# Optimization experiments

Hardware: AMD Instinct MI355X
Metric: run time of the kernel (lower is better)

The kernel has to match this reference:

```python
import jax, jax.numpy as jnp
import numpy as np
import math

B, LQ, LK = 8, 1024, 1024
D_MODEL, NHEAD = 512, 8
DH = D_MODEL // NHEAD
FACTOR = 5
U = FACTOR * int(np.ceil(np.log(LQ)))  # 35: Informer's sample_k == n_top here (L_Q == L_K)


def _ln(x, g, b, eps=1e-5):
    m = x.mean(-1, keepdims=True)
    v = ((x - m) ** 2).mean(-1, keepdims=True)
    return (x - m) / jnp.sqrt(v + eps) * g + b


def _heads(x):  # (B,L,D) -> (B,H,L,Dh)
    Bx, L, _ = x.shape
    return x.reshape(Bx, L, NHEAD, DH).transpose(0, 2, 1, 3)


def _merge(x):  # (B,H,L,Dh) -> (B,L,D)
    Bx, H, L, Dh = x.shape
    return x.transpose(0, 2, 1, 3).reshape(Bx, L, H * Dh)


def _prob_attn(q, k, v, index_sample):
    # Informer ProbAttention, mask_flag=False. q,k,v: (B,H,L,Dh)
    Bx, H, Lq, Dh = q.shape
    Lk = k.shape[2]
    k_samp = k[:, :, index_sample, :]                        # (B,H,Lq,U,Dh) gathered keys
    qk_samp = jnp.einsum('bhld,bhlud->bhlu', q, k_samp)      # sampled scores
    M = qk_samp.max(-1) - qk_samp.sum(-1) / Lk               # sparsity measurement (B,H,Lq)
    _, top = jax.lax.top_k(M, U)                             # (B,H,U) top-u query indices
    q_red = jnp.take_along_axis(q, top[..., None], axis=2)   # (B,H,U,Dh)
    scores = jnp.einsum('bhud,bhkd->bhuk', q_red, k) * (1.0 / math.sqrt(Dh))
    attn = jax.nn.softmax(scores, axis=-1)
    upd = jnp.einsum('bhuk,bhkd->bhud', attn, v)             # (B,H,U,Dh)
    # initial context = mean of V (non-causal branch), then scatter top-u rows
    ctx = jnp.broadcast_to(v.mean(2, keepdims=True), (Bx, H, Lq, Dh))
    bi = jnp.arange(Bx)[:, None, None]
    hi = jnp.arange(H)[None, :, None]
    ctx = ctx.at[bi, hi, top].set(upd)
    return ctx


def _full_attn(q, k, v):
    s = jnp.einsum('bhld,bhsd->bhls', q, k) * (1.0 / math.sqrt(q.shape[-1]))
    a = jax.nn.softmax(s, axis=-1)
    return jnp.einsum('bhls,bhsd->bhld', a, v)


def setup_inputs():
    key = jax.random.key(0)
    ks = jax.random.split(key, 40)
    d = {}
    d['tgt'] = jax.random.normal(ks[0], (B, LQ, D_MODEL), jnp.float32)
    d['memory'] = jax.random.normal(ks[1], (B, LK, D_MODEL), jnp.float32)
    d['index_sample'] = jax.random.randint(ks[2], (LQ, U), 0, LK)
    i = 3
    for pre in ('1', '2'):
        for n in ('q', 'k', 'v', 'o'):
            d['w%s%s' % (n, pre)] = jax.random.normal(ks[i], (D_MODEL, D_MODEL), jnp.float32) * 0.02
            d['b%s%s' % (n, pre)] = jnp.zeros((D_MODEL,), jnp.float32)
            i += 1
    d['conv1_w'] = jax.random.normal(ks[i], (D_MODEL, 4 * D_MODEL), jnp.float32) * 0.02; i += 1
    d['conv1_b'] = jnp.zeros((4 * D_MODEL,), jnp.float32)
    d['conv2_w'] = jax.random.normal(ks[i], (4 * D_MODEL, D_MODEL), jnp.float32) * 0.02; i += 1
    d['conv2_b'] = jnp.zeros((D_MODEL,), jnp.float32)
    for n in ('ln1', 'ln2', 'ln3'):
        d[n + '_g'] = jnp.ones((D_MODEL,), jnp.float32)
        d[n + '_b'] = jnp.zeros((D_MODEL,), jnp.float32)
    return d


def reference(tgt, memory, index_sample, wq1, bq1, wk1, bk1, wv1, bv1, wo1, bo1,
              wq2, bq2, wk2, bk2, wv2, bv2, wo2, bo2,
              conv1_w, conv1_b, conv2_w, conv2_b,
              ln1_g, ln1_b, ln2_g, ln2_b, ln3_g, ln3_b):
    # dropout layers are identity (eval mode)
    x = tgt
    q = _heads(x @ wq1 + bq1)
    k = _heads(x @ wk1 + bk1)
    v = _heads(x @ wv1 + bv1)
    xn = _merge(_prob_attn(q, k, v, index_sample)) @ wo1 + bo1   # ProbSparse self-attn
    x = _ln(x + xn, ln1_g, ln1_b)                                # norm_enc1, with residual
    q = _heads(x @ wq2 + bq2)
    k = _heads(memory @ wk2 + bk2)
    v = _heads(memory @ wv2 + bv2)
    x = _merge(_full_attn(q, k, v)) @ wo2 + bo2                  # full cross-attn (no residual, per source)
    y = x = _ln(x, ln2_g, ln2_b)                                 # norm_enc2
    y = jax.nn.relu(y @ conv1_w + conv1_b) @ conv2_w + conv2_b   # conv1x1 FFN
    return _ln(x + y, ln3_g, ln3_b)                              # norm_enc3
```

## Files before the change

kernel.cpp:

```cpp
#include <hip/hip_runtime.h>
#include <hip/hip_bf16.h>
#include <cstdint>

constexpr int Bb  = 8;
constexpr int Ls  = 1024;
constexpr int DM  = 512;
constexpr int NH  = 8;
constexpr int DHd = 64;
constexpr int MR  = Bb * Ls;
constexpr int ZH  = Bb * NH;

typedef __attribute__((ext_vector_type(8))) short short8v;
typedef __attribute__((ext_vector_type(4))) short short4v;
typedef __attribute__((ext_vector_type(4))) float floatx4;

__device__ inline short f2bf(float x) {
  __hip_bfloat16 h = __float2bfloat16(x);
  return *reinterpret_cast<short*>(&h);
}
__device__ inline float bf2f(short s) {
  return __uint_as_float(((uint32_t)(uint16_t)s) << 16);
}

#define GLOAD_LDS16(g, l)                                                        \
  __builtin_amdgcn_global_load_lds(                                              \
      (const __attribute__((address_space(1))) void*)(g),                        \
      (__attribute__((address_space(3))) void*)(l), 16, 0, 0)

template<int MODE, int RELU>
__global__ __launch_bounds__(256) void k_gemm_mfma(
    const __hip_bfloat16* __restrict__ A, const __hip_bfloat16* __restrict__ Wt,
    const float* __restrict__ bias, const float* __restrict__ bias1,
    const float* __restrict__ bias2,
    void* __restrict__ Cout, void* __restrict__ aux1, void* __restrict__ aux2,
    void* __restrict__ aux3,
    int M, int N, int K)
{
  __shared__ __hip_bfloat16 As[128 * 32];
  __shared__ __hip_bfloat16 Bs[128 * 32];
  const int tid = threadIdx.x;
  const int w = tid >> 6, lane = tid & 63;
  const int wr = w >> 1, wc = w & 1;
  const int bm = blockIdx.x * 128, bn = blockIdx.y * 128;
  const int lrow = lane >> 2;
  const int lcol = (lane & 3) * 8;
  const int fr = lane & 15;
  const int fco = (lane >> 4) * 8;
  const short* Ash = (const short*)As;
  const short* Bsh = (const short*)Bs;

  const __hip_bfloat16* Asrc = A;
  if (MODE == 12 && bn >= 512) Asrc = (const __hip_bfloat16*)aux3;

  const int ksl = K / gridDim.z;
  const int kb0 = blockIdx.z * ksl;

  floatx4 acc[4][4] = {};
  for (int k0 = kb0; k0 < kb0 + ksl; k0 += 32) {
#pragma unroll
    for (int i = 0; i < 2; ++i) {
      const int chunk = w * 2 + i;
      GLOAD_LDS16(Asrc + (size_t)(bm + chunk * 16 + lrow) * K + k0 + lcol,
                  As + chunk * 512);
      GLOAD_LDS16(Wt + (size_t)(bn + chunk * 16 + lrow) * K + k0 + lcol,
                  Bs + chunk * 512);
    }
    __syncthreads();
    short8v a[4], b[4];
#pragma unroll
    for (int mi = 0; mi < 4; ++mi)
      a[mi] = *(const short8v*)(Ash + (wr * 64 + mi * 16 + fr) * 32 + fco);
#pragma unroll
    for (int ni = 0; ni < 4; ++ni)
      b[ni] = *(const short8v*)(Bsh + (wc * 64 + ni * 16 + fr) * 32 + fco);
#pragma unroll
    for (int mi = 0; mi < 4; ++mi)
#pragma unroll
      for (int ni = 0; ni < 4; ++ni)
        acc[mi][ni] = __builtin_amdgcn_mfma_f32_16x16x32_bf16(
            a[mi], b[ni], acc[mi][ni], 0, 0, 0);
    __syncthreads();
  }
#pragma unroll
  for (int ni = 0; ni < 4; ++ni) {
    const int cn = bn + wc * 64 + ni * 16 + fr;
    float bv = 0.f;
    if (MODE == 10 || MODE == 12) {
      const float* bp = (cn < 512) ? bias : (cn < 1024 ? bias1 : bias2);
      bv = bp[cn & 511];
    } else if (MODE != 20) {
      bv = bias[cn];
    }
#pragma unroll
    for (int mi = 0; mi < 4; ++mi) {
#pragma unroll
      for (int j = 0; j < 4; ++j) {
        const int rm = bm + wr * 64 + mi * 16 + (lane >> 4) * 4 + j;
        float v = acc[mi][ni][j] + bv;
        if (RELU) v = fmaxf(v, 0.f);
        if (MODE == 1) {
          ((__hip_bfloat16*)Cout)[(size_t)rm * N + cn] = __float2bfloat16(v);
        } else if (MODE == 10) {
          const int sel = cn >> 9, c = cn & 511;
          if (sel == 2) {
            ((float*)aux2)[(size_t)rm * 512 + c] = v;
          } else {
            const int bb = rm >> 10, l = rm & 1023, hh = c >> 6, dd = c & 63;
            const size_t ci = (((size_t)(bb * 8 + hh)) * 1024 + l) * 64 + dd;
            float* base = sel ? (float*)aux1 : (float*)Cout;
            base[ci] = v;
            __hip_bfloat16* bb16 = (__hip_bfloat16*)aux3 +
                                   (sel ? (size_t)ZH * Ls * 64 : 0);
            bb16[ci] = __float2bfloat16(v);
          }
        } else if (MODE == 12) {
          const int sel = cn >> 9, c = cn & 511;
          if (sel == 0) {
            ((__hip_bfloat16*)Cout)[(size_t)rm * 512 + c] =
                __float2bfloat16(v * 0.125f);
          } else if (sel == 1) {
            const int cs = (c & ~63) | ((c & 63) ^ ((rm & 7) << 3));
            ((__hip_bfloat16*)aux1)[(size_t)rm * 512 + cs] = __float2bfloat16(v);
          } else {
            const int bb = rm >> 10, l = rm & 1023, hh = c >> 6, dd = c & 63;
            ((__hip_bfloat16*)aux2)[(size_t)((bb * 8 + hh) * 64 + dd) * 1024 +
                                    (l ^ ((dd & 7) << 3))] = __float2bfloat16(v);
          }
        } else if (MODE == 20) {
          float* pz = (float*)(blockIdx.z == 0 ? Cout :
                      blockIdx.z == 1 ? aux1 :
                      blockIdx.z == 2 ? aux2 : aux3);
          pz[(size_t)rm * N + cn] = v;
        }
      }
    }
  }
}

__global__ __launch_bounds__(512) void k_flash2(
    const __hip_bfloat16* __restrict__ Qb,
    const __hip_bfloat16* __restrict__ Kb,
    const __hip_bfloat16* __restrict__ Vt,
    __hip_bfloat16* __restrict__ O)
{
  __shared__ __hip_bfloat16 Ks[2][64 * 64];
  __shared__ __hip_bfloat16 Vs[2][64 * 64];
  __shared__ __hip_bfloat16 Ps[8 * 16 * 72];
  const int tid = threadIdx.x, w = tid >> 6, lane = tid & 63;
  const int g = lane >> 4, r = lane & 15;
  const int z = blockIdx.y, b = z >> 3, h = z & 7;
  const int q0 = blockIdx.x * 128 + w * 16;
  __hip_bfloat16* Pw = Ps + w * 16 * 72;

  const int srow = w * 8 + (lane >> 3);
  const int sseg = lane & 7;

  const short8v qf0 = *(const short8v*)(Qb + (size_t)(b * Ls + q0 + r) * DM + h * DHd + g * 8);
  const short8v qf1 = *(const short8v*)(Qb + (size_t)(b * Ls + q0 + r) * DM + h * DHd + 32 + g * 8);

  floatx4 oacc[4] = {};
  float m_run = -1e30f, l_run = 0.f;

  GLOAD_LDS16(Kb + (size_t)(b * Ls + srow) * DM + h * DHd + sseg * 8, &Ks[0][w * 512]);
  GLOAD_LDS16(Vt + ((size_t)z * DHd + srow) * Ls + sseg * 8, &Vs[0][w * 512]);
  asm volatile("s_waitcnt vmcnt(0)" ::: "memory");
  __builtin_amdgcn_s_barrier();

  int cur = 0;
  for (int t = 0; t < 16; ++t) {
    if (t + 1 < 16) {
      GLOAD_LDS16(Kb + (size_t)(b * Ls + (t + 1) * 64 + srow) * DM + h * DHd + sseg * 8,
                  &Ks[cur ^ 1][w * 512]);
      GLOAD_LDS16(Vt + ((size_t)z * DHd + srow) * Ls + (t + 1) * 64 + sseg * 8,
                  &Vs[cur ^ 1][w * 512]);
    }
    const __hip_bfloat16* Kc = Ks[cur];
    const __hip_bfloat16* Vc = Vs[cur];
    float sv[4][4];
    float tmax = -1e30f;
    __builtin_amdgcn_s_setprio(1);
#pragma unroll
    for (int kt = 0; kt < 4; ++kt) {
      const int key = kt * 16 + r, sw = key & 7;
      short8v a0 = *(const short8v*)(Kc + key * 64 + ((g ^ sw) * 8));
      short8v a1 = *(const short8v*)(Kc + key * 64 + (((4 + g) ^ sw) * 8));
      floatx4 c = {};
      c = __builtin_amdgcn_mfma_f32_16x16x32_bf16(a0, qf0, c, 0, 0, 0);
      c = __builtin_amdgcn_mfma_f32_16x16x32_bf16(a1, qf1, c, 0, 0, 0);
#pragma unroll
      for (int j = 0; j < 4; ++j) {
        float x = c[j];
        sv[kt][j] = x;
        tmax = fmaxf(tmax, x);
      }
    }
    __builtin_amdgcn_s_setprio(0);
    tmax = fmaxf(tmax, __shfl_xor(tmax, 16));
    tmax = fmaxf(tmax, __shfl_xor(tmax, 32));
    float m_new;
    if (__all(tmax <= m_run + 8.0f)) {
      m_new = m_run;
    } else {
      m_new = fmaxf(m_run, tmax);
      const float fac = __expf(m_run - m_new);
      float fj[4];
#pragma unroll
      for (int j = 0; j < 4; ++j) fj[j] = __shfl(fac, (lane & 48) | (g * 4 + j));
#pragma unroll
      for (int ct = 0; ct < 4; ++ct)
#pragma unroll
        for (int j = 0; j < 4; ++j) oacc[ct][j] *= fj[j];
      l_run *= fac;
    }
    float psum = 0.f;
#pragma unroll
    for (int kt = 0; kt < 4; ++kt) {
      short4v pk;
#pragma unroll
      for (int j = 0; j < 4; ++j) {
        float p = __expf(sv[kt][j] - m_new);
        psum += p;
        pk[j] = f2bf(p);
      }
      *(short4v*)(Pw + r * 72 + kt * 16 + g * 4) = pk;
    }
    psum += __shfl_xor(psum, 16);
    psum += __shfl_xor(psum, 32);
    l_run += psum;
    m_run = m_new;
    const short8v pa0 = *(const short8v*)(Pw + r * 72 + g * 8);
    const short8v pa1 = *(const short8v*)(Pw + r * 72 + 32 + g * 8);
    __builtin_amdgcn_s_setprio(1);
#pragma unroll
    for (int ct = 0; ct < 4; ++ct) {
      const int d = ct * 16 + r, sw = d & 7;
      short8v v0 = *(const short8v*)(Vc + d * 64 + ((g ^ sw) * 8));
      short8v v1 = *(const short8v*)(Vc + d * 64 + (((4 + g) ^ sw) * 8));
      oacc[ct] = __builtin_amdgcn_mfma_f32_16x16x32_bf16(pa0, v0, oacc[ct], 0, 0, 0);
      oacc[ct] = __builtin_amdgcn_mfma_f32_16x16x32_bf16(pa1, v1, oacc[ct], 0, 0, 0);
    }
    __builtin_amdgcn_s_setprio(0);
    asm volatile("s_waitcnt vmcnt(0)" ::: "memory");
    __builtin_amdgcn_s_barrier();
    cur ^= 1;
  }
  float li[4];
#pragma unroll
  for (int j = 0; j < 4; ++j)
    li[j] = 1.0f / __shfl(l_run, (lane & 48) | (g * 4 + j));
#pragma unroll
  for (int ct = 0; ct < 4; ++ct)
#pragma unroll
    for (int j = 0; j < 4; ++j)
      O[(size_t)(b * Ls + q0 + g * 4 + j) * DM + h * DHd + ct * 16 + r] =
          __float2bfloat16(oacc[ct][j] * li[j]);
}

struct CvtArgs { const float* s[12]; __hip_bfloat16* d[12]; };
__global__ __launch_bounds__(256) void k_cvt_all(CvtArgs a)
{
  const int bid = blockIdx.x, tid = threadIdx.x;
  if (bid < 8192) {
    const size_t half = (size_t)MR * DM / 4;
    size_t i = (size_t)bid * 256 + tid;
    const float* in = a.s[10]; __hip_bfloat16* out = a.d[10];
    if (i >= half) { i -= half; in = a.s[11]; out = a.d[11]; }
    float4 v = *reinterpret_cast<const float4*>(in + i * 4);
    short4v o;
    o.x = f2bf(v.x); o.y = f2bf(v.y); o.z = f2bf(v.z); o.w = f2bf(v.w);
    *reinterpret_cast<short4v*>(out + i * 4) = o;
    return;
  }
  __shared__ float t[32][33];
  const int wb = bid - 8192;
  int widx, K, N, kblk, nblk;
  if (wb < 2048) {
    widx = wb >> 8; const int w2 = wb & 255;
    K = 512; N = 512; kblk = w2 & 15; nblk = w2 >> 4;
  } else if (wb < 3072) {
    widx = 8; const int w2 = wb - 2048;
    K = 512; N = 2048; kblk = w2 & 15; nblk = w2 >> 4;
  } else {
    widx = 9; const int w2 = wb - 3072;
    K = 2048; N = 512; kblk = w2 & 63; nblk = w2 >> 6;
  }
  const float* W = a.s[widx];
  __hip_bfloat16* Wt = a.d[widx];
  const int k0 = kblk * 32, n0 = nblk * 32;
  const int r = tid >> 3, c = (tid & 7) * 4;
  float4 v = *reinterpret_cast<const float4*>(W + (size_t)(k0 + r) * N + n0 + c);
  t[r][c + 0] = v.x; t[r][c + 1] = v.y; t[r][c + 2] = v.z; t[r][c + 3] = v.w;
  __syncthreads();
  short4v o;
  o.x = f2bf(t[c + 0][r]); o.y = f2bf(t[c + 1][r]);
  o.z = f2bf(t[c + 2][r]); o.w = f2bf(t[c + 3][r]);
  *reinterpret_cast<short4v*>(Wt + (size_t)(n0 + r) * K + k0 + c) = o;
}

__global__ __launch_bounds__(256) void k_probflash(
    const float* __restrict__ Qz, const float* __restrict__ Kz,
    const float* __restrict__ Vm, const int* __restrict__ top,
    float* __restrict__ Op, float* __restrict__ Ml, float* __restrict__ Ll,
    int U)
{
  __shared__ float Qs[DHd][64 + 4];
  __shared__ float Ks[DHd][64 + 4];
  __shared__ float Vs[64][64];
  const int bid = blockIdx.x;
  const int swz = (bid & 7) * ((16 * ZH) >> 3) + (bid >> 3);
  const int kc = swz & 15, z = swz >> 4, b = z >> 3, h = z & 7;
  const int tid = threadIdx.x;
  const int k0 = kc * 64;
#pragma unroll
  for (int i = 0; i < 4; ++i) {
    const int idx = tid + (i << 8);
    const int r = idx >> 4, c4 = (idx & 15) << 2;
    int u = r; if (u >= U) u = U - 1;
    const int qr = top[z * U + u];
    float4 q4 = *reinterpret_cast<const float4*>(Qz + ((size_t)z * Ls + qr) * 64 + c4);
    Qs[c4 + 0][r] = q4.x; Qs[c4 + 1][r] = q4.y; Qs[c4 + 2][r] = q4.z; Qs[c4 + 3][r] = q4.w;
    float4 k4 = *reinterpret_cast<const float4*>(Kz + ((size_t)z * Ls + k0 + r) * 64 + c4);
    Ks[c4 + 0][r] = k4.x; Ks[c4 + 1][r] = k4.y; Ks[c4 + 2][r] = k4.z; Ks[c4 + 3][r] = k4.w;
    *reinterpret_cast<float4*>(&Vs[r][c4]) =
        *reinterpret_cast<const float4*>(Vm + ((size_t)(b * Ls + k0 + r)) * DM + h * DHd + c4);
  }
  __syncthreads();
  const int mB = (tid >> 4) << 2, nB = (tid & 15) << 2;
  float acc[4][4] = {};
#pragma unroll
  for (int kk = 0; kk < DHd; ++kk) {
    float4 a4 = *reinterpret_cast<const float4*>(&Qs[kk][mB]);
    float4 b4 = *reinterpret_cast<const float4*>(&Ks[kk][nB]);
    const float av[4] = {a4.x, a4.y, a4.z, a4.w};
#pragma unroll
    for (int i = 0; i < 4; ++i) {
      acc[i][0] += av[i] * b4.x; acc[i][1] += av[i] * b4.y;
      acc[i][2] += av[i] * b4.z; acc[i][3] += av[i] * b4.w;
    }
  }
  __syncthreads();
  float (*Ss)[68] = (float (*)[68])Qs;
#pragma unroll
  for (int i = 0; i < 4; ++i) {
    float4 o;
    o.x = acc[i][0] * 0.125f; o.y = acc[i][1] * 0.125f;
    o.z = acc[i][2] * 0.125f; o.w = acc[i][3] * 0.125f;
    *reinterpret_cast<float4*>(&Ss[mB + i][nB]) = o;
  }
  __syncthreads();
  {
    const int row = tid >> 2, q = tid & 3;
    float mx = -1e30f;
#pragma unroll
    for (int j = 0; j < 16; ++j) mx = fmaxf(mx, Ss[row][q * 16 + j]);
    mx = fmaxf(mx, __shfl_xor(mx, 1));
    mx = fmaxf(mx, __shfl_xor(mx, 2));
    float se = 0.f;
#pragma unroll
    for (int j = 0; j < 16; ++j) {
      float p = __expf(Ss[row][q * 16 + j] - mx);
      Ss[row][q * 16 + j] = p;
      se += p;
    }
    se += __shfl_xor(se, 1);
    se += __shfl_xor(se, 2);
    if (q == 0) {
      Ml[((size_t)kc * ZH + z) * 64 + row] = mx;
      Ll[((size_t)kc * ZH + z) * 64 + row] = se;
    }
  }
  __syncthreads();
  const int d = tid & 63, w = tid >> 6;
  float acc2[16] = {};
  for (int k = 0; k < 64; ++k) {
    const float vk = Vs[k][d];
#pragma unroll
    for (int i = 0; i < 16; ++i)
      acc2[i] += Ss[w * 16 + i][k] * vk;
  }
  float* outb = Op + ((size_t)kc * ZH + z) * 4096;
#pragma unroll
  for (int i = 0; i < 16; ++i)
    outb[(w * 16 + i) * 64 + d] = acc2[i];
}

__global__ __launch_bounds__(256) void k_prob_comb(
    const float* __restrict__ Op, const float* __restrict__ Ml,
    const float* __restrict__ Ll, const int* __restrict__ top,
    __hip_bfloat16* __restrict__ ctx, int U)
{
  __shared__ float wsh[16][64];
  __shared__ float Lsh[64];
  const int z = blockIdx.x, b = z >> 3, h = z & 7;
  const int tid = threadIdx.x;
  if (tid < 64) {
    float M = -1e30f;
#pragma unroll
    for (int c = 0; c < 16; ++c)
      M = fmaxf(M, Ml[((size_t)c * ZH + z) * 64 + tid]);
    float L = 0.f;
#pragma unroll
    for (int c = 0; c < 16; ++c) {
      float wv = __expf(Ml[((size_t)c * ZH + z) * 64 + tid] - M);
      wsh[c][tid] = wv;
      L += wv * Ll[((size_t)c * ZH + z) * 64 + tid];
    }
    Lsh[tid] = L;
  }
  __syncthreads();
  for (int e = tid; e < U * 64; e += 256) {
    const int u = e >> 6, d = e & 63;
    float s = 0.f;
#pragma unroll
    for (int c = 0; c < 16; ++c)
      s += wsh[c][u] * Op[((size_t)c * ZH + z) * 4096 + u * 64 + d];
    const int row = top[z * U + u];
    ctx[((size_t)(b * Ls + row)) * DM + h * DHd + d] =
        __float2bfloat16(s / Lsh[u]);
  }
}

template<int UU>
__global__ __launch_bounds__(256) void k_mscore4(
    const __hip_bfloat16* __restrict__ Qzb, const __hip_bfloat16* __restrict__ Kzb,
    const int* __restrict__ smp, float* __restrict__ Ms)
{
  const int bid = blockIdx.x;
  const int swz = (bid & 7) * 256 + (bid >> 3);
  const int gw = swz * 4 + (threadIdx.x >> 6);
  const int lane = threadIdx.x & 63;
  const int li = lane >> 3, dp = (lane & 7) * 8;
  const int l = (gw & 127) * 8 + li;
  const int z = gw >> 7;
  const short8v q8 = *(const short8v*)(Qzb + ((size_t)z * Ls + l) * 64 + dp);
  float qf[8];
#pragma unroll
  for (int j = 0; j < 8; ++j) qf[j] = bf2f(q8[j]);
  int kidx[UU];
#pragma unroll
  for (int u = 0; u < UU; ++u) kidx[u] = smp[l * UU + u];
  const __hip_bfloat16* kzb = Kzb + (size_t)z * Ls * 64 + dp;
  float mx = -1e30f, sm = 0.f;
#pragma unroll
  for (int u = 0; u < UU; ++u) {
    const short8v k8 = *(const short8v*)(kzb + (size_t)kidx[u] * 64);
    float d = qf[0] * bf2f(k8[0]) + qf[1] * bf2f(k8[1])
            + qf[2] * bf2f(k8[2]) + qf[3] * bf2f(k8[3])
            + qf[4] * bf2f(k8[4]) + qf[5] * bf2f(k8[5])
            + qf[6] * bf2f(k8[6]) + qf[7] * bf2f(k8[7]);
    d += __shfl_xor(d, 1);
    d += __shfl_xor(d, 2);
    d += __shfl_xor(d, 4);
    mx = fmaxf(mx, d);
    sm += d;
  }
  if ((lane & 7) == 0) Ms[z * Ls + l] = mx - sm * (1.0f / Ls);
}

__global__ __launch_bounds__(256) void k_mscore4g(
    const __hip_bfloat16* __restrict__ Qzb, const __hip_bfloat16* __restrict__ Kzb,
    const int* __restrict__ smp, float* __restrict__ Ms, int U)
{
  const int bid = blockIdx.x;
  const int swz = (bid & 7) * 256 + (bid >> 3);
  const int gw = swz * 4 + (threadIdx.x >> 6);
  const int lane = threadIdx.x & 63;
  const int li = lane >> 3, dp = (lane & 7) * 8;
  const int l = (gw & 127) * 8 + li;
  const int z = gw >> 7;
  const short8v q8 = *(const short8v*)(Qzb + ((size_t)z * Ls + l) * 64 + dp);
  float qf[8];
#pragma unroll
  for (int j = 0; j < 8; ++j) qf[j] = bf2f(q8[j]);
  const __hip_bfloat16* kzb = Kzb + (size_t)z * Ls * 64 + dp;
  float mx = -1e30f, sm = 0.f;
  for (int u = 0; u < U; ++u) {
    const short8v k8 = *(const short8v*)(kzb + (size_t)smp[l * U + u] * 64);
    float d = qf[0] * bf2f(k8[0]) + qf[1] * bf2f(k8[1])
            + qf[2] * bf2f(k8[2]) + qf[3] * bf2f(k8[3])
            + qf[4] * bf2f(k8[4]) + qf[5] * bf2f(k8[5])
            + qf[6] * bf2f(k8[6]) + qf[7] * bf2f(k8[7]);
    d += __shfl_xor(d, 1);
    d += __shfl_xor(d, 2);
    d += __shfl_xor(d, 4);
    mx = fmaxf(mx, d);
    sm += d;
  }
  if ((lane & 7) == 0) Ms[z * Ls + l] = mx - sm * (1.0f / Ls);
}

__global__ __launch_bounds__(64) void k_topk_w(
    const float* __restrict__ Ms, int* __restrict__ top, int U)
{
  const int z = blockIdx.x, lane = threadIdx.x;
  float v[16];
#pragma unroll
  for (int j = 0; j < 16; ++j) v[j] = Ms[z * Ls + j * 64 + lane];
  for (int it = 0; it < U; ++it) {
    float bv = -1e30f; int bi = 0x7fffffff;
#pragma unroll
    for (int j = 0; j < 16; ++j) {
      const int idx = j * 64 + lane;
      if (v[j] > bv) { bv = v[j]; bi = idx; }
    }
#pragma unroll
    for (int off = 1; off < 64; off <<= 1) {
      const float ov = __shfl_xor(bv, off);
      const int   oi = __shfl_xor(bi, off);
      if (ov > bv || (ov == bv && oi < bi)) { bv = ov; bi = oi; }
    }
    if (lane == 0) top[z * U + it] = bi;
    if ((bi & 63) == lane) v[bi >> 6] = -1e30f;
  }
}

__global__ __launch_bounds__(256) void k_meanv1(
    const float* __restrict__ Vm, float* __restrict__ mvp)
{
  __shared__ float ps[4][64];
  const int gid = blockIdx.x, z = gid >> 3, c = gid & 7, b = z >> 3, h = z & 7;
  const int d = threadIdx.x & 63, g = threadIdx.x >> 6;
  float s = 0.f;
  const int kb = c * 128 + g * 32;
  for (int k = kb; k < kb + 32; ++k)
    s += Vm[((size_t)(b * Ls + k)) * DM + h * DHd + d];
  ps[g][d] = s;
  __syncthreads();
  if (g == 0) mvp[(z * 8 + c) * 64 + d] = ps[0][d] + ps[1][d] + ps[2][d] + ps[3][d];
}

__global__ __launch_bounds__(256) void k_ctxfillb(
    const float* __restrict__ mvp, __hip_bfloat16* __restrict__ ctx)
{
  const int i = blockIdx.x * 256 + threadIdx.x;
  const int c4 = (i & 127) << 2;
  const int row = i >> 7;
  const int b = row >> 10;
  const int h = c4 >> 6;
  const float* base = mvp + ((b * 8 + h) * 8) * 64 + (c4 & 63);
  float4 a = {0.f, 0.f, 0.f, 0.f};
#pragma unroll
  for (int c = 0; c < 8; ++c) {
    float4 m4 = *reinterpret_cast<const float4*>(base + c * 64);
    a.x += m4.x; a.y += m4.y; a.z += m4.z; a.w += m4.w;
  }
  const float inv = 1.0f / Ls;
  short4v o;
  o.x = f2bf(a.x * inv); o.y = f2bf(a.y * inv);
  o.z = f2bf(a.z * inv); o.w = f2bf(a.w * inv);
  *reinterpret_cast<short4v*>(ctx + (size_t)row * DM + c4) = o;
}

template<int NP>
__global__ __launch_bounds__(256) void k_ln2(
    const float* __restrict__ x0, const float* __restrict__ x1,
    const float* __restrict__ x2, const float* __restrict__ x3,
    const float* __restrict__ res, const float* __restrict__ bias,
    const float* __restrict__ g, const float* __restrict__ be,
    float* __restrict__ outf, __hip_bfloat16* __restrict__ outb)
{
  __shared__ float red[4];
  const int row = blockIdx.x, tid = threadIdx.x;
  const size_t base = (size_t)row * DM;
  float2 v = *reinterpret_cast<const float2*>(x0 + base + tid * 2);
  if (NP > 1) {
    float2 a = *reinterpret_cast<const float2*>(x1 + base + tid * 2);
    v.x += a.x; v.y += a.y;
  }
  if (NP > 2) {
    float2 a = *reinterpret_cast<const float2*>(x2 + base + tid * 2);
    v.x += a.x; v.y += a.y;
  }
  if (NP > 3) {
    float2 a = *reinterpret_cast<const float2*>(x3 + base + tid * 2);
    v.x += a.x; v.y += a.y;
  }
  if (bias) {
    float2 a = *reinterpret_cast<const float2*>(bias + tid * 2);
    v.x += a.x; v.y += a.y;
  }
  if (res) {
    float2 r2 = *reinterpret_cast<const float2*>(res + base + tid * 2);
    v.x += r2.x; v.y += r2.y;
  }
  float s = v.x + v.y;
#pragma unroll
  for (int off = 32; off; off >>= 1) s += __shfl_xor(s, off);
  if ((tid & 63) == 0) red[tid >> 6] = s;
  __syncthreads();
  s = red[0] + red[1] + red[2] + red[3];
  const float mean = s * (1.0f / DM);
  __syncthreads();
  float dx = v.x - mean, dy = v.y - mean;
  float q = dx * dx + dy * dy;
#pragma unroll
  for (int off = 32; off; off >>= 1) q += __shfl_xor(q, off);
  if ((tid & 63) == 0) red[tid >> 6] = q;
  __syncthreads();
  q = red[0] + red[1] + red[2] + red[3];
  const float inv = rsqrtf(q * (1.0f / DM) + 1e-5f);
  float2 gg = *reinterpret_cast<const float2*>(g + tid * 2);
  float2 bb = *reinterpret_cast<const float2*>(be + tid * 2);
  float ox = dx * inv * gg.x + bb.x;
  float oy = dy * inv * gg.y + bb.y;
  if (outf) {
    float2 o; o.x = ox; o.y = oy;
    *reinterpret_cast<float2*>(outf + base + tid * 2) = o;
  }
  if (outb) {
    short2 ob; ob.x = f2bf(ox); ob.y = f2bf(oy);
    *reinterpret_cast<short2*>(outb + base + tid * 2) = ob;
  }
}

extern "C" void kernel_launch(void* const* d_in, const int* in_sizes, int n_in,
                              void* d_out, int out_size, void* d_ws, size_t ws_size,
                              hipStream_t stream)
{
  const float* tgt = (const float*)d_in[0];
  const float* mem = (const float*)d_in[1];
  const int*   smp = (const int*)d_in[2];
  const float* wq1 = (const float*)d_in[3];  const float* bq1 = (const float*)d_in[4];
  const float* wk1 = (const float*)d_in[5];  const float* bk1 = (const float*)d_in[6];
  const float* wv1 = (const float*)d_in[7];  const float* bv1 = (const float*)d_in[8];
  const float* wo1 = (const float*)d_in[9];  const float* bo1 = (const float*)d_in[10];
  const float* wq2 = (const float*)d_in[11]; const float* bq2 = (const float*)d_in[12];
  const float* wk2 = (const float*)d_in[13]; const float* bk2 = (const float*)d_in[14];
  const float* wv2 = (const float*)d_in[15]; const float* bv2 = (const float*)d_in[16];
  const float* wo2 = (const float*)d_in[17]; const float* bo2 = (const float*)d_in[18];
  const float* c1w = (const float*)d_in[19]; const float* c1b = (const float*)d_in[20];
  const float* c2w = (const float*)d_in[21]; const float* c2b = (const float*)d_in[22];
  const float* g1  = (const float*)d_in[23]; const float* be1 = (const float*)d_in[24];
  const float* g2  = (const float*)d_in[25]; const float* be2 = (const float*)d_in[26];
  const float* g3  = (const float*)d_in[27]; const float* be3 = (const float*)d_in[28];
  float* outp = (float*)d_out;

  const int U   = in_sizes[2] / Ls;

  char* ws = (char*)d_ws;
  const size_t SZ = (size_t)MR * DM * sizeof(float);
  float* Qz   = (float*)(ws);
  float* Kz   = (float*)(ws + SZ);
  float* W0   = Qz;
  float* W1   = Kz;
  float* W2   = (float*)(ws + 2 * SZ);
  float* Sbuf = (float*)(ws + 3 * SZ);
  float* Op   = Sbuf + (size_t)ZH * 64 * Ls;
  __hip_bfloat16* QKzb = (__hip_bfloat16*)Sbuf;
  __hip_bfloat16* Qzb = QKzb;
  __hip_bfloat16* Kzb = QKzb + (size_t)ZH * Ls * 64;
  __hip_bfloat16* Tb  = (__hip_bfloat16*)(ws + 5 * SZ);
  __hip_bfloat16* Mb  = (__hip_bfloat16*)(ws + 5 * SZ + SZ / 2);
  __hip_bfloat16* Xb  = (__hip_bfloat16*)(ws + 6 * SZ);
  __hip_bfloat16* Vtb = (__hip_bfloat16*)(ws + 6 * SZ + SZ / 2);
  __hip_bfloat16* Wt3 = Vtb;
  float* CP2 = (float*)(ws + 5 * SZ);
  float* CP3 = (float*)(ws + 6 * SZ);
  char* tail = ws + 7 * SZ;
  __hip_bfloat16* wo1b = (__hip_bfloat16*)tail; tail += DM * DM * 2;
  __hip_bfloat16* wq2b = (__hip_bfloat16*)tail; tail += DM * DM * 2;
  __hip_bfloat16* wk2b = (__hip_bfloat16*)tail; tail += DM * DM * 2;
  __hip_bfloat16* wv2b = (__hip_bfloat16*)tail; tail += DM * DM * 2;
  __hip_bfloat16* wo2b = (__hip_bfloat16*)tail; tail += DM * DM * 2;
  __hip_bfloat16* c1wb = (__hip_bfloat16*)tail; tail += DM * 4 * DM * 2;
  __hip_bfloat16* c2wb = (__hip_bfloat16*)tail; tail += DM * 4 * DM * 2;
  float* Ms  = (float*)tail; tail += (size_t)ZH * Ls * 4;
  int*   top = (int*)tail;   tail += (size_t)ZH * 64 * 4;
  float* mvp = (float*)tail; tail += (size_t)ZH * 8 * DHd * 4;
  float* Ml  = (float*)tail; tail += (size_t)16 * ZH * 64 * 4;
  float* Ll  = (float*)tail; tail += (size_t)16 * ZH * 64 * 4;
  __hip_bfloat16* Kb = Tb;
  __hip_bfloat16* Qb = (__hip_bfloat16*)d_out;
  __hip_bfloat16* hb = (__hip_bfloat16*)Sbuf;

  CvtArgs ca;
  ca.s[0] = wq1; ca.d[0] = Wt3;
  ca.s[1] = wk1; ca.d[1] = Wt3 + DM * DM;
  ca.s[2] = wv1; ca.d[2] = Wt3 + 2 * DM * DM;
  ca.s[3] = wo1; ca.d[3] = wo1b;
  ca.s[4] = wq2; ca.d[4] = wq2b;
  ca.s[5] = wk2; ca.d[5] = wk2b;
  ca.s[6] = wv2; ca.d[6] = wv2b;
  ca.s[7] = wo2; ca.d[7] = wo2b;
  ca.s[8] = c1w; ca.d[8] = c1wb;
  ca.s[9] = c2w; ca.d[9] = c2wb;
  ca.s[10] = tgt; ca.d[10] = Tb;
  ca.s[11] = mem; ca.d[11] = Mb;
  k_cvt_all<<<dim3(12288), 256, 0, stream>>>(ca);

  k_gemm_mfma<10, 0><<<dim3(MR / 128, 12), 256, 0, stream>>>(
      Tb, Wt3, bq1, bk1, bv1, Qz, Kz, W2, QKzb, MR, 1536, DM);

  if (U == 35)
    k_mscore4<35><<<dim3(2048), 256, 0, stream>>>(Qzb, Kzb, smp, Ms);
  else
    k_mscore4g<<<dim3(2048), 256, 0, stream>>>(Qzb, Kzb, smp, Ms, U);
  k_topk_w<<<dim3(ZH), 64, 0, stream>>>(Ms, top, U);
  k_probflash<<<dim3(16 * ZH), 256, 0, stream>>>(Qz, Kz, W2, top, Op, Ml, Ll, U);
  k_meanv1<<<dim3(ZH * 8), 256, 0, stream>>>(W2, mvp);
  k_ctxfillb<<<dim3(MR * DM / 4 / 256), 256, 0, stream>>>(mvp, Xb);
  k_prob_comb<<<dim3(ZH), 256, 0, stream>>>(Op, Ml, Ll, top, Xb, U);

  k_gemm_mfma<20, 0><<<dim3(MR / 128, DM / 128, 2), 256, 0, stream>>>(
      Xb, wo1b, nullptr, nullptr, nullptr, W0, W1, nullptr, nullptr, MR, DM, DM);
  k_ln2<2><<<dim3(MR), 256, 0, stream>>>(W0, W1, nullptr, nullptr,
                                         tgt, bo1, g1, be1, nullptr, Xb);

  k_gemm_mfma<12, 0><<<dim3(MR / 128, 12), 256, 0, stream>>>(
      Xb, wq2b, bq2, bk2, bv2, Qb, Kb, Vtb, (void*)Mb, MR, 1536, DM);

  k_flash2<<<dim3(Ls / 128, ZH), 512, 0, stream>>>(Qb, Kb, Vtb, Xb);

  k_gemm_mfma<20, 0><<<dim3(MR / 128, DM / 128, 2), 256, 0, stream>>>(
      Xb, wo2b, nullptr, nullptr, nullptr, W0, W2, nullptr, nullptr, MR, DM, DM);
  k_ln2<2><<<dim3(MR), 256, 0, stream>>>(W0, W2, nullptr, nullptr,
                                         nullptr, bo2, g2, be2, W1, Xb);

  k_gemm_mfma<1, 1><<<dim3(MR / 128, 4 * DM / 128), 256, 0, stream>>>(
      Xb, c1wb, c1b, nullptr, nullptr, hb, nullptr, nullptr, nullptr, MR, 4 * DM, DM);
  k_gemm_mfma<20, 0><<<dim3(MR / 128, DM / 128, 4), 256, 0, stream>>>(
      hb, c2wb, nullptr, nullptr, nullptr, W0, W2, CP2, CP3, MR, DM, 2 * DM * 2);
  k_ln2<4><<<dim3(MR), 256, 0, stream>>>(W0, W2, CP2, CP3,
                                         W1, c2b, g3, be3, outp, nullptr);
}
```

Before: 345.5 us.

## Double-buffer MFMA GEMM LDS tiles and fuse V-mean/ctx fill into prob-attention kernels

The GEMM kernel now uses two LDS buffers and prefetches the next K-slice while computing on the current one, with one barrier per step instead of two. This is meant to hide global-load latency behind MFMA work. Separately, the V column mean is computed inside k_probflash from the V tile already in LDS, and the ctx mean fill moves into the combine kernel, which removes two launches and a re-read of V. The cost is double the LDS per GEMM block, which may lower occupancy. The combine kernel now writes the whole ctx slice from only 64 blocks, so that fill may serialize.

Result: faster. 332.4 us (-3.8%).

```diff
diff --git a/kernel.cpp b/kernel.cpp
--- a/kernel.cpp
+++ b/kernel.cpp
@@ -36,8 +36,8 @@
     void* __restrict__ aux3,
     int M, int N, int K)
 {
-  __shared__ __hip_bfloat16 As[128 * 32];
-  __shared__ __hip_bfloat16 Bs[128 * 32];
+  __shared__ __hip_bfloat16 As[2][128 * 32];
+  __shared__ __hip_bfloat16 Bs[2][128 * 32];
   const int tid = threadIdx.x;
   const int w = tid >> 6, lane = tid & 63;
   const int wr = w >> 1, wc = w & 1;
@@ -46,26 +46,42 @@
   const int lcol = (lane & 3) * 8;
   const int fr = lane & 15;
   const int fco = (lane >> 4) * 8;
-  const short* Ash = (const short*)As;
-  const short* Bsh = (const short*)Bs;
 
   const __hip_bfloat16* Asrc = A;
   if (MODE == 12 && bn >= 512) Asrc = (const __hip_bfloat16*)aux3;
 
   const int ksl = K / gridDim.z;
   const int kb0 = blockIdx.z * ksl;
+  const int nst = ksl / 32;
+
+  const int chunk0 = w * 2, chunk1 = w * 2 + 1;
+  const size_t aoff0 = (size_t)(bm + chunk0 * 16 + lrow) * K + lcol;
+  const size_t aoff1 = (size_t)(bm + chunk1 * 16 + lrow) * K + lcol;
+  const size_t boff0 = (size_t)(bn + chunk0 * 16 + lrow) * K + lcol;
+  const size_t boff1 = (size_t)(bn + chunk1 * 16 + lrow) * K + lcol;
+
+  {
+    const int k0 = kb0;
+    GLOAD_LDS16(Asrc + aoff0 + k0, &As[0][chunk0 * 512]);
+    GLOAD_LDS16(Asrc + aoff1 + k0, &As[0][chunk1 * 512]);
+    GLOAD_LDS16(Wt + boff0 + k0, &Bs[0][chunk0 * 512]);
+    GLOAD_LDS16(Wt + boff1 + k0, &Bs[0][chunk1 * 512]);
+  }
+  asm volatile("s_waitcnt vmcnt(0)" ::: "memory");
+  __builtin_amdgcn_s_barrier();
 
   floatx4 acc[4][4] = {};
-  for (int k0 = kb0; k0 < kb0 + ksl; k0 += 32) {
-#pragma unroll
-    for (int i = 0; i < 2; ++i) {
-      const int chunk = w * 2 + i;
-      GLOAD_LDS16(Asrc + (size_t)(bm + chunk * 16 + lrow) * K + k0 + lcol,
-                  As + chunk * 512);
-      GLOAD_LDS16(Wt + (size_t)(bn + chunk * 16 + lrow) * K + k0 + lcol,
-                  Bs + chunk * 512);
-    }
-    __syncthreads();
+  int cur = 0;
+  for (int t = 0; t < nst; ++t) {
+    if (t + 1 < nst) {
+      const int k0 = kb0 + (t + 1) * 32;
+      GLOAD_LDS16(Asrc + aoff0 + k0, &As[cur ^ 1][chunk0 * 512]);
+      GLOAD_LDS16(Asrc + aoff1 + k0, &As[cur ^ 1][chunk1 * 512]);
+      GLOAD_LDS16(Wt + boff0 + k0, &Bs[cur ^ 1][chunk0 * 512]);
+      GLOAD_LDS16(Wt + boff1 + k0, &Bs[cur ^ 1][chunk1 * 512]);
+    }
+    const short* Ash = (const short*)As[cur];
+    const short* Bsh = (const short*)Bs[cur];
     short8v a[4], b[4];
 #pragma unroll
     for (int mi = 0; mi < 4; ++mi)
@@ -79,7 +95,9 @@
       for (int ni = 0; ni < 4; ++ni)
         acc[mi][ni] = __builtin_amdgcn_mfma_f32_16x16x32_bf16(
             a[mi], b[ni], acc[mi][ni], 0, 0, 0);
-    __syncthreads();
+    asm volatile("s_waitcnt vmcnt(0)" ::: "memory");
+    __builtin_amdgcn_s_barrier();
+    cur ^= 1;
   }
 #pragma unroll
   for (int ni = 0; ni < 4; ++ni) {
@@ -301,11 +319,12 @@
     const float* __restrict__ Qz, const float* __restrict__ Kz,
     const float* __restrict__ Vm, const int* __restrict__ top,
     float* __restrict__ Op, float* __restrict__ Ml, float* __restrict__ Ll,
-    int U)
+    float* __restrict__ mvp, int U)
 {
   __shared__ float Qs[DHd][64 + 4];
   __shared__ float Ks[DHd][64 + 4];
   __shared__ float Vs[64][64];
+  __shared__ float ps[4][64];
   const int bid = blockIdx.x;
   const int swz = (bid & 7) * ((16 * ZH) >> 3) + (bid >> 3);
   const int kc = swz & 15, z = swz >> 4, b = z >> 3, h = z & 7;
@@ -371,6 +390,12 @@
   }
   __syncthreads();
   const int d = tid & 63, w = tid >> 6;
+  {
+    float s = 0.f;
+#pragma unroll
+    for (int i = 0; i < 16; ++i) s += Vs[w * 16 + i][d];
+    ps[w][d] = s;
+  }
   float acc2[16] = {};
   for (int k = 0; k < 64; ++k) {
     const float vk = Vs[k][d];
@@ -382,15 +407,19 @@
 #pragma unroll
   for (int i = 0; i < 16; ++i)
     outb[(w * 16 + i) * 64 + d] = acc2[i];
-}
-
-__global__ __launch_bounds__(256) void k_prob_comb(
+  __syncthreads();
+  if (w == 0)
+    mvp[((size_t)z * 16 + kc) * 64 + d] = ps[0][d] + ps[1][d] + ps[2][d] + ps[3][d];
+}
+
+__global__ __launch_bounds__(256) void k_prob_comb2(
     const float* __restrict__ Op, const float* __restrict__ Ml,
     const float* __restrict__ Ll, const int* __restrict__ top,
-    __hip_bfloat16* __restrict__ ctx, int U)
+    const float* __restrict__ mvp, __hip_bfloat16* __restrict__ ctx, int U)
 {
   __shared__ float wsh[16][64];
   __shared__ float Lsh[64];
+  __shared__ short4v mvb[16];
   const int z = blockIdx.x, b = z >> 3, h = z & 7;
   const int tid = threadIdx.x;
   if (tid < 64) {
@@ -406,6 +435,17 @@
       L += wv * Ll[((size_t)c * ZH + z) * 64 + tid];
     }
     Lsh[tid] = L;
+    float s = 0.f;
+#pragma unroll
+    for (int c = 0; c < 16; ++c) s += mvp[((size_t)z * 16 + c) * 64 + tid];
+    const short mb = f2bf(s * (1.0f / Ls));
+    ((short*)mvb)[tid] = mb;
+  }
+  __syncthreads();
+  __hip_bfloat16* base = ctx + (size_t)(b * Ls) * DM + h * DHd;
+  for (int i = tid; i < 1024 * 16; i += 256) {
+    const int row = i >> 4, c4 = i & 15;
+    *reinterpret_cast<short4v*>(base + (size_t)row * DM + c4 * 4) = mvb[c4];
   }
   __syncthreads();
   for (int e = tid; e < U * 64; e += 256) {
@@ -512,43 +552,6 @@
     if (lane == 0) top[z * U + it] = bi;
     if ((bi & 63) == lane) v[bi >> 6] = -1e30f;
   }
-}
-
-__global__ __launch_bounds__(256) void k_meanv1(
-    const float* __restrict__ Vm, float* __restrict__ mvp)
-{
-  __shared__ float ps[4][64];
-  const int gid = blockIdx.x, z = gid >> 3, c = gid & 7, b = z >> 3, h = z & 7;
-  const int d = threadIdx.x & 63, g = threadIdx.x >> 6;
-  float s = 0.f;
-  const int kb = c * 128 + g * 32;
-  for (int k = kb; k < kb + 32; ++k)
-    s += Vm[((size_t)(b * Ls + k)) * DM + h * DHd + d];
-  ps[g][d] = s;
-  __syncthreads();
-  if (g == 0) mvp[(z * 8 + c) * 64 + d] = ps[0][d] + ps[1][d] + ps[2][d] + ps[3][d];
-}
-
-__global__ __launch_bounds__(256) void k_ctxfillb(
-    const float* __restrict__ mvp, __hip_bfloat16* __restrict__ ctx)
-{
-  const int i = blockIdx.x * 256 + threadIdx.x;
-  const int c4 = (i & 127) << 2;
-  const int row = i >> 7;
-  const int b = row >> 10;
-  const int h = c4 >> 6;
-  const float* base = mvp + ((b * 8 + h) * 8) * 64 + (c4 & 63);
-  float4 a = {0.f, 0.f, 0.f, 0.f};
-#pragma unroll
-  for (int c = 0; c < 8; ++c) {
-    float4 m4 = *reinterpret_cast<const float4*>(base + c * 64);
-    a.x += m4.x; a.y += m4.y; a.z += m4.z; a.w += m4.w;
-  }
-  const float inv = 1.0f / Ls;
-  short4v o;
-  o.x = f2bf(a.x * inv); o.y = f2bf(a.y * inv);
-  o.z = f2bf(a.z * inv); o.w = f2bf(a.w * inv);
-  *reinterpret_cast<short4v*>(ctx + (size_t)row * DM + c4) = o;
 }
 
 template<int NP>
@@ -666,7 +669,7 @@
   __hip_bfloat16* c2wb = (__hip_bfloat16*)tail; tail += DM * 4 * DM * 2;
   float* Ms  = (float*)tail; tail += (size_t)ZH * Ls * 4;
   int*   top = (int*)tail;   tail += (size_t)ZH * 64 * 4;
-  float* mvp = (float*)tail; tail += (size_t)ZH * 8 * DHd * 4;
+  float* mvp = (float*)tail; tail += (size_t)ZH * 16 * DHd * 4;
   float* Ml  = (float*)tail; tail += (size_t)16 * ZH * 64 * 4;
   float* Ll  = (float*)tail; tail += (size_t)16 * ZH * 64 * 4;
   __hip_bfloat16* Kb = Tb;
@@ -696,10 +699,8 @@
   else
     k_mscore4g<<<dim3(2048), 256, 0, stream>>>(Qzb, Kzb, smp, Ms, U);
   k_topk_w<<<dim3(ZH), 64, 0, stream>>>(Ms, top, U);
-  k_probflash<<<dim3(16 * ZH), 256, 0, stream>>>(Qz, Kz, W2, top, Op, Ml, Ll, U);
-  k_meanv1<<<dim3(ZH * 8), 256, 0, stream>>>(W2, mvp);
-  k_ctxfillb<<<dim3(MR * DM / 4 / 256), 256, 0, stream>>>(mvp, Xb);
-  k_prob_comb<<<dim3(ZH), 256, 0, stream>>>(Op, Ml, Ll, top, Xb, U);
+  k_probflash<<<dim3(16 * ZH), 256, 0, stream>>>(Qz, Kz, W2, top, Op, Ml, Ll, mvp, U);
+  k_prob_comb2<<<dim3(ZH), 256, 0, stream>>>(Op, Ml, Ll, top, mvp, Xb, U);
 
   k_gemm_mfma<20, 0><<<dim3(MR / 128, DM / 128, 2), 256, 0, stream>>>(
       Xb, wo1b, nullptr, nullptr, nullptr, W0, W1, nullptr, nullptr, MR, DM, DM);
```
